# Kernel optimization log

Hardware: AMD Instinct MI355X
Metric: run time of the kernel (lower is better)

The kernel has to match this reference:

```python
import jax, jax.numpy as jnp
import numpy as np
from fractions import Fraction
from math import factorial, sqrt

# ---------- e3nn-convention real Wigner 3j, unit Frobenius norm ----------
def _su2_cg(j1, m1, j2, m2, j3, m3):
    if m3 != m1 + m2:
        return 0.0
    f = lambda n: factorial(int(n))
    vmin = int(max(-j1 + j2 + m3, -j1 + m1, 0))
    vmax = int(min(j2 + j3 + m1, j3 - j1 + j2, j3 + m3))
    C = ((2.0 * j3 + 1.0) * Fraction(
        f(j3 + j1 - j2) * f(j3 - j1 + j2) * f(j1 + j2 - j3) * f(j3 + m3) * f(j3 - m3),
        f(j1 + j2 + j3 + 1) * f(j1 - m1) * f(j1 + m1) * f(j2 - m2) * f(j2 + m2))) ** 0.5
    S = Fraction(0)
    for v in range(vmin, vmax + 1):
        S += (-1) ** int(v + j2 + m2) * Fraction(
            f(j2 + j3 + m1 - v) * f(j1 - m1 + v),
            f(v) * f(j3 - j1 + j2 - v) * f(j3 + m3 - v) * f(v + j1 - j2 - m3))
    return float(C) * float(S)

def _q(l):  # real->complex spherical-harmonic change of basis (e3nn convention)
    q = np.zeros((2 * l + 1, 2 * l + 1), dtype=np.complex128)
    for m in range(-l, 0):
        q[l + m, l + abs(m)] = 1 / 2 ** 0.5
        q[l + m, l - abs(m)] = -1j / 2 ** 0.5
    q[l, l] = 1
    for m in range(1, l + 1):
        q[l + m, l + abs(m)] = (-1) ** m / 2 ** 0.5
        q[l + m, l - abs(m)] = 1j * (-1) ** m / 2 ** 0.5
    return (-1j) ** l * q

def wigner_3j(l1, l2, l3):
    cg = np.zeros((2 * l1 + 1, 2 * l2 + 1, 2 * l3 + 1))
    for m1 in range(-l1, l1 + 1):
        for m2 in range(-l2, l2 + 1):
            if abs(m1 + m2) <= l3:
                cg[l1 + m1, l2 + m2, l3 + m1 + m2] = _su2_cg(l1, m1, l2, m2, l3, m1 + m2)
    C = np.einsum('ij,kl,mn,ikn->jlm', _q(l1), _q(l2), np.conj(_q(l3).T), cg.astype(np.complex128))
    C = np.real(C)
    return (C / np.linalg.norm(C)).astype(np.float32)

# ---------- TensorProduct config: 32x0e+32x1o+32x2e (x) same -> same, all uvw paths ----------
MUL = 32
LS = (0, 1, 2)
OFF = (0, MUL * 1, MUL * 1 + MUL * 3)  # block offsets in the flat 288-dim layout
DIM = MUL * (1 + 3 + 5)                # 288
INS = [(0, 0, 0), (1, 1, 0), (2, 2, 0),
       (0, 1, 1), (1, 0, 1), (1, 2, 1), (2, 1, 1),
       (0, 2, 2), (1, 1, 2), (2, 0, 2), (2, 2, 2)]
_counts = {io: sum(1 for i in INS if i[2] == io) for io in set(i[2] for i in INS)}
# 'component' normalization: scale unit-norm w3j by sqrt(2*l_out+1); uvw mode: alpha=sqrt(path_weight/(n_paths_to_out*mul1*mul2))
ALPHA = [sqrt((2 * LS[io] + 1) / (_counts[io] * MUL * MUL)) for (_, _, io) in INS]
W3J = {(LS[i1], LS[i2], LS[io]): wigner_3j(LS[i1], LS[i2], LS[io]) for (i1, i2, io) in INS}


def setup_inputs() -> dict:
    key = jax.random.key(0)
    k1, k2, k3 = jax.random.split(key, 3)
    B = 2048
    return {
        'x1': jax.random.normal(k1, (B, DIM), dtype=jnp.float32),
        'x2': jax.random.normal(k2, (B, DIM), dtype=jnp.float32),
        'ws': jax.random.normal(k3, (len(INS), MUL, MUL, MUL), dtype=jnp.float32),
    }


def reference(x1, x2, ws):
    B = x1.shape[0]
    out = jnp.zeros((B, DIM), dtype=x1.dtype)
    for p, (i1, i2, io) in enumerate(INS):
        l1, l2, lo = LS[i1], LS[i2], LS[io]
        s1 = x1[:, OFF[i1]:OFF[i1] + MUL * (2 * l1 + 1)].reshape(B, MUL, 2 * l1 + 1)
        s2 = x2[:, OFF[i2]:OFF[i2] + MUL * (2 * l2 + 1)].reshape(B, MUL, 2 * l2 + 1)
        C = jnp.asarray(W3J[(l1, l2, lo)], dtype=x1.dtype)
        # z u v w: batch, mul_in1, mul_in2, mul_out ; i j k: 2l+1 components
        r = jnp.einsum('uvw,ijk,zui,zvj->zwk', ws[p], C, s1, s2)
        out = out.at[:, OFF[io]:OFF[io] + MUL * (2 * lo + 1)].add(ALPHA[p] * r.reshape(B, -1))
    return out
```

## Files before the change

### kernel.cpp

```cpp
#include <hip/hip_runtime.h>
#include <hip/hip_bf16.h>
#include <cmath>
#include <complex>
#include <algorithm>


typedef std::complex<double> cd;

static double factd(int n) { double r = 1; for (int i = 2; i <= n; ++i) r *= i; return r; }

static double su2_cg(int j1, int m1, int j2, int m2, int j3, int m3) {
    if (m3 != m1 + m2) return 0.0;
    int vmin = std::max(std::max(-j1 + j2 + m3, -j1 + m1), 0);
    int vmax = std::min(std::min(j2 + j3 + m1, j3 - j1 + j2), j3 + m3);
    double C = std::sqrt((2.0 * j3 + 1.0) *
        (factd(j3 + j1 - j2) * factd(j3 - j1 + j2) * factd(j1 + j2 - j3) *
         factd(j3 + m3) * factd(j3 - m3)) /
        (factd(j1 + j2 + j3 + 1) * factd(j1 - m1) * factd(j1 + m1) *
         factd(j2 - m2) * factd(j2 + m2)));
    double S = 0.0;
    for (int v = vmin; v <= vmax; ++v) {
        double sgn = ((v + j2 + m2) & 1) ? -1.0 : 1.0;
        S += sgn * (factd(j2 + j3 + m1 - v) * factd(j1 - m1 + v)) /
             (factd(v) * factd(j3 - j1 + j2 - v) * factd(j3 + m3 - v) *
              factd(v + j1 - j2 - m3));
    }
    return C * S;
}

static void qmat(int l, cd* q) {
    int n = 2 * l + 1;
    for (int i = 0; i < n * n; ++i) q[i] = cd(0, 0);
    const double s = 1.0 / std::sqrt(2.0);
    for (int m = -l; m < 0; ++m) {
        q[(l + m) * n + (l - m)] = cd(s, 0);
        q[(l + m) * n + (l + m)] = cd(0, -s);
    }
    q[l * n + l] = cd(1, 0);
    for (int m = 1; m <= l; ++m) {
        double sg = (m & 1) ? -1.0 : 1.0;
        q[(l + m) * n + (l + m)] = cd(sg * s, 0);
        q[(l + m) * n + (l - m)] = cd(0, sg * s);
    }
    cd ph(1, 0);
    for (int t = 0; t < l; ++t) ph *= cd(0, -1);
    for (int i = 0; i < n * n; ++i) q[i] *= ph;
}

static void wigner3j_dense(int l1, int l2, int l3, double* outp) {
    int n1 = 2 * l1 + 1, n2 = 2 * l2 + 1, n3 = 2 * l3 + 1;
    double cg[125];
    for (int i = 0; i < n1 * n2 * n3; ++i) cg[i] = 0.0;
    for (int m1 = -l1; m1 <= l1; ++m1)
        for (int m2 = -l2; m2 <= l2; ++m2) {
            int m3 = m1 + m2;
            if (std::abs(m3) <= l3)
                cg[((l1 + m1) * n2 + (l2 + m2)) * n3 + (l3 + m3)] =
                    su2_cg(l1, m1, l2, m2, l3, m3);
        }
    cd q1[25], q2[25], q3[25];
    qmat(l1, q1); qmat(l2, q2); qmat(l3, q3);
    double norm2 = 0.0;
    for (int j = 0; j < n1; ++j)
        for (int l = 0; l < n2; ++l)
            for (int m = 0; m < n3; ++m) {
                cd sum(0, 0);
                for (int i = 0; i < n1; ++i)
                    for (int k = 0; k < n2; ++k)
                        for (int n = 0; n < n3; ++n) {
                            double g = cg[(i * n2 + k) * n3 + n];
                            if (g != 0.0)
                                sum += q1[i * n1 + j] * q2[k * n2 + l] *
                                       std::conj(q3[n * n3 + m]) * g;
                        }
                outp[(j * n2 + l) * n3 + m] = sum.real();
                norm2 += sum.real() * sum.real();
            }
    double inv = 1.0 / std::sqrt(norm2);
    for (int t = 0; t < n1 * n2 * n3; ++t) outp[t] *= inv;
}


struct E3 { unsigned char i, j, k; };

constexpr E3 PAT_P0[1]  = {{0,0,0}};
constexpr E3 PAT_P1[3]  = {{0,0,0},{1,1,0},{2,2,0}};
constexpr E3 PAT_P2[5]  = {{0,0,0},{1,1,0},{2,2,0},{3,3,0},{4,4,0}};
constexpr E3 PAT_P3[3]  = {{0,0,0},{0,1,1},{0,2,2}};
constexpr E3 PAT_P4[3]  = {{0,0,0},{1,0,1},{2,0,2}};
constexpr E3 PAT_P5[11] = {{1,2,1},{1,3,2},{1,1,0},{2,2,2},{0,2,0},{2,3,1},
                           {0,1,1},{2,4,2},{0,0,2},{2,0,0},{0,4,0}};
constexpr E3 PAT_P6[11] = {{2,1,1},{2,2,2},{2,0,0},{3,1,2},{1,1,0},{3,2,1},
                           {1,0,1},{4,2,2},{0,0,2},{4,0,0},{0,2,0}};
constexpr E3 PAT_P7[5]  = {{0,0,0},{0,1,1},{0,2,2},{0,3,3},{0,4,4}};
constexpr E3 PAT_P8[11] = {{1,1,2},{1,2,3},{1,0,1},{2,1,3},{0,1,1},{2,2,2},
                           {0,0,2},{2,2,4},{0,0,4},{2,0,0},{0,2,0}};
constexpr E3 PAT_P9[5]  = {{0,0,0},{1,0,1},{2,0,2},{3,0,3},{4,0,4}};
constexpr E3 PAT_P10[25]= {{2,2,2},{2,3,3},{2,1,1},{2,4,4},{2,0,0},{3,2,3},
                           {1,2,1},{3,3,2},{1,1,2},{3,3,4},{1,1,4},{3,1,0},
                           {1,3,0},{3,4,3},{1,0,3},{3,0,1},{1,4,1},{4,2,4},
                           {0,2,0},{4,3,3},{0,1,3},{4,1,1},{0,3,1},{4,4,2},
                           {0,0,2}};

constexpr int OFF_P[11] = {0, 1, 4, 9, 12, 15, 26, 37, 42, 53, 58};

struct W3JArg { float c[83]; };

static W3JArg build_w3j_sparse() {
    struct PD { const E3* pat; int ne; int l1, l2, lo; double alpha; };
    const double a0 = std::sqrt(1.0/3072.0), a1 = std::sqrt(3.0/4096.0),
                 a2 = std::sqrt(5.0/4096.0);
    const PD pd[11] = {
        {PAT_P0, 1, 0,0,0, a0}, {PAT_P1, 3, 1,1,0, a0}, {PAT_P2, 5, 2,2,0, a0},
        {PAT_P3, 3, 0,1,1, a1}, {PAT_P4, 3, 1,0,1, a1}, {PAT_P5,11, 1,2,1, a1},
        {PAT_P6,11, 2,1,1, a1}, {PAT_P7, 5, 0,2,2, a2}, {PAT_P8,11, 1,1,2, a2},
        {PAT_P9, 5, 2,0,2, a2}, {PAT_P10,25,2,2,2, a2}
    };
    W3JArg arg;
    for (int p = 0; p < 11; ++p) {
        double dense[125];
        wigner3j_dense(pd[p].l1, pd[p].l2, pd[p].lo, dense);
        int n2 = 2*pd[p].l2+1, n3 = 2*pd[p].lo+1;
        for (int e = 0; e < pd[p].ne; ++e) {
            const E3& t = pd[p].pat[e];
            arg.c[OFF_P[p] + e] =
                (float)(dense[(t.i * n2 + t.j) * n3 + t.k] * pd[p].alpha);
        }
    }
    return arg;
}


typedef __attribute__((ext_vector_type(8))) short short8;
typedef __attribute__((ext_vector_type(4))) float f32x4;

__device__ __forceinline__ unsigned short f2bf_bits(float f) {
    __hip_bfloat16 h = __float2bfloat16(f);
    unsigned short u; __builtin_memcpy(&u, &h, 2); return u;
}

__device__ __forceinline__ unsigned pack2(float lo, float hi) {
    float2 f2; f2.x = lo; f2.y = hi;
    __hip_bfloat162 pk = __float22bfloat162_rn(f2);
    unsigned u; __builtin_memcpy(&u, &pk, 4); return u;
}

template<int NE, int A1, int A2, int D3, int SBASE, int SSTR>
__device__ __forceinline__ void do_path(const E3 (&pat)[NE],
                                        const float* __restrict__ cs,
                                        const float* a, const float* b0,
                                        const float* b1,
                                        unsigned* __restrict__ dst) {
    float ca[NE];
    #pragma unroll
    for (int e = 0; e < NE; ++e) ca[e] = cs[e] * a[A1 + pat[e].i];
    float t0[D3], t1[D3];
    #pragma unroll
    for (int k = 0; k < D3; ++k) { t0[k] = 0.0f; t1[k] = 0.0f; }
    #pragma unroll
    for (int e = 0; e < NE; ++e) {
        const int k = pat[e].k;
        t0[k] = fmaf(ca[e], b0[A2 + pat[e].j], t0[k]);
        t1[k] = fmaf(ca[e], b1[A2 + pat[e].j], t1[k]);
    }
    #pragma unroll
    for (int k = 0; k < D3; ++k)
        dst[(SBASE + k * SSTR) * 256] = pack2(t0[k], t1[k]);
}

__device__ __forceinline__ void build_all(const float* __restrict__ cs,
                                          const float* a, const float* b0,
                                          const float* b1,
                                          unsigned* __restrict__ dst) {
    do_path< 1,0,0,1, 0,1>(PAT_P0,  cs +  0, a, b0, b1, dst);
    do_path< 3,1,1,1, 1,1>(PAT_P1,  cs +  1, a, b0, b1, dst);
    do_path< 5,4,4,1, 2,1>(PAT_P2,  cs +  4, a, b0, b1, dst);
    do_path< 3,0,1,3, 3,4>(PAT_P3,  cs +  9, a, b0, b1, dst);
    do_path< 3,1,0,3, 4,4>(PAT_P4,  cs + 12, a, b0, b1, dst);
    do_path<11,1,4,3, 5,4>(PAT_P5,  cs + 15, a, b0, b1, dst);
    do_path<11,4,1,3, 6,4>(PAT_P6,  cs + 26, a, b0, b1, dst);
    do_path< 5,0,4,5,15,4>(PAT_P7,  cs + 37, a, b0, b1, dst);
    do_path<11,1,1,5,16,4>(PAT_P8,  cs + 42, a, b0, b1, dst);
    do_path< 5,4,0,5,17,4>(PAT_P9,  cs + 53, a, b0, b1, dst);
    do_path<25,4,4,5,18,4>(PAT_P10, cs + 58, a, b0, b1, dst);
}

__device__ __forceinline__ void load_a(const float* __restrict__ x1r, int u,
                                       float* a) {
    a[0] = x1r[u];
    #pragma unroll
    for (int i = 0; i < 3; ++i) a[1 + i] = x1r[32 + u * 3 + i];
    #pragma unroll
    for (int i = 0; i < 5; ++i) a[4 + i] = x1r[128 + u * 5 + i];
}

template<bool USE_WST>
__device__ __forceinline__ short8 load_bfrag(const float* __restrict__ ws,
                                             const unsigned short* __restrict__ wsT,
                                             int p, int u, int w, int vbase) {
    if constexpr (USE_WST) {
        return *(const short8*)(wsT + (((size_t)(p*32+u)*32 + w)*32 + vbase));
    } else {
        short8 r;
        #pragma unroll
        for (int j = 0; j < 8; ++j) {
            float f = ws[((size_t)(p*32+u)*32 + (vbase+j))*32 + w];
            r[j] = (short)f2bf_bits(f);
        }
        return r;
    }
}

__global__ void ws_prep(const float* __restrict__ ws,
                        unsigned short* __restrict__ wsT) {
    __shared__ float tile[32][33];
    const int pu = blockIdx.x, tid = threadIdx.x;
    const float4 f = ((const float4*)(ws + (size_t)pu * 1024))[tid];
    const int v = tid >> 3, w0 = (tid & 7) * 4;
    tile[v][w0+0] = f.x; tile[v][w0+1] = f.y; tile[v][w0+2] = f.z; tile[v][w0+3] = f.w;
    __syncthreads();
    const int w = tid >> 3, vB = (tid & 7) * 4;
    ushort4 o;
    o.x = f2bf_bits(tile[vB+0][w]); o.y = f2bf_bits(tile[vB+1][w]);
    o.z = f2bf_bits(tile[vB+2][w]); o.w = f2bf_bits(tile[vB+3][w]);
    *(ushort4*)(wsT + (size_t)pu * 1024 + tid * 4) = o;
}


__launch_bounds__(256, 4)
__global__ void tp_mfma(const float* __restrict__ x1,
                        const float* __restrict__ x2,
                        const unsigned short* __restrict__ wsT,
                        float* __restrict__ part, int ZT, W3JArg w3j) {
    __shared__ unsigned shT[35 * 256];

    const int tid = threadIdx.x;
    const int l = tid & 63, wv = tid >> 6, kh = wv & 1, nt = wv >> 1;
    const int zt = blockIdx.x & (ZT - 1);
    const int ug = blockIdx.x / ZT;
    const int z0 = zt * 16, u0 = ug * 4;
    const int tz = tid >> 4, vp = tid & 15, v0 = vp * 2;

    float b0[9], b1[9];
    {
        const float* xr = x2 + (size_t)(z0 + tz) * 288;
        float2 s0 = *(const float2*)(xr + v0);
        b0[0] = s0.x; b1[0] = s0.y;
        const float* p1 = xr + 32 + v0 * 3;
        float2 q0 = *(const float2*)(p1 + 0);
        float2 q1 = *(const float2*)(p1 + 2);
        float2 q2 = *(const float2*)(p1 + 4);
        b0[1] = q0.x; b0[2] = q0.y; b0[3] = q1.x;
        b1[1] = q1.y; b1[2] = q2.x; b1[3] = q2.y;
        const float* p2 = xr + 128 + v0 * 5;
        #pragma unroll
        for (int h = 0; h < 5; ++h) {
            float2 r = *(const float2*)(p2 + 2 * h);
            if (2 * h < 5) b0[4 + 2 * h] = r.x; else b1[4 + 2 * h - 5] = r.x;
            if (2 * h + 1 < 5) b0[5 + 2 * h] = r.y; else b1[4 + 2 * h - 4] = r.y;
        }
    }

    const float* x1r = x1 + (size_t)(z0 + tz) * 288;

    unsigned* dstT = shT + tz * 16 + (vp & 3) + ((((vp >> 2) + (tz >> 1)) & 3) << 2);
    const unsigned* tbase = shT + (l & 15) * 16 +
                            ((((l >> 4) + ((l & 15) >> 1)) & 3) << 2);

    const int w  = (l & 15) + nt * 16;
    const int vb = (l >> 4) * 8;

    f32x4 acc[5];
    #pragma unroll
    for (int i = 0; i < 5; ++i) acc[i] = (f32x4)(0.0f);

    float a[2][9];
    load_a(x1r, u0, a[0]);

    for (int ui = 0; ui < 4; ++ui) {
        const int u = u0 + ui;
        const int cur = ui & 1;

        __syncthreads();

        short8 bf[7];
        if (kh == 0) {
            #pragma unroll
            for (int p = 0; p < 7; ++p) bf[p] = load_bfrag<true>(nullptr, wsT, p, u, w, vb);
        } else {
            #pragma unroll
            for (int p = 0; p < 4; ++p) bf[p] = load_bfrag<true>(nullptr, wsT, 7 + p, u, w, vb);
        }
        if (ui < 3) load_a(x1r, u + 1, a[cur ^ 1]);

        build_all(w3j.c, a[cur], b0, b1, dstT);
        __syncthreads();

        if (kh == 0) {
            #pragma unroll
            for (int m = 0; m < 3; ++m) {
                short8 af = *(const short8*)(tbase + m * 256);
                acc[0] = __builtin_amdgcn_mfma_f32_16x16x32_bf16(af, bf[m], acc[0], 0, 0, 0);
            }
            #pragma unroll
            for (int g = 0; g < 3; ++g)
                #pragma unroll
                for (int m = 0; m < 4; ++m) {
                    short8 af = *(const short8*)(tbase + (3 + g*4 + m) * 256);
                    acc[1+g] = __builtin_amdgcn_mfma_f32_16x16x32_bf16(af, bf[3+m], acc[1+g], 0, 0, 0);
                }
        } else {
            #pragma unroll
            for (int g = 0; g < 5; ++g)
                #pragma unroll
                for (int m = 0; m < 4; ++m) {
                    short8 af = *(const short8*)(tbase + (15 + g*4 + m) * 256);
                    acc[g] = __builtin_amdgcn_mfma_f32_16x16x32_bf16(af, bf[m], acc[g], 0, 0, 0);
                }
        }
    }

    float* pb = part + ((size_t)(ug * ZT + zt) * 9) * 512;
    const int zi4 = (l >> 4) << 2;
    if (kh == 0) {
        #pragma unroll
        for (int r = 0; r < 4; ++r)
            pb[(zi4 + r) * 32 + w] = acc[0][r];
        #pragma unroll
        for (int k = 0; k < 3; ++k)
            #pragma unroll
            for (int r = 0; r < 4; ++r)
                pb[(1 + k) * 512 + (zi4 + r) * 32 + w] = acc[1 + k][r];
    } else {
        #pragma unroll
        for (int k = 0; k < 5; ++k)
            #pragma unroll
            for (int r = 0; r < 4; ++r)
                pb[(4 + k) * 512 + (zi4 + r) * 32 + w] = acc[k][r];
    }
}


__global__ void reduce_out(const float* __restrict__ part,
                           float* __restrict__ out, int ZT) {
    const int bid = blockIdx.x;
    const int zt = bid / 9, comp = bid - zt * 9;
    const int tid = threadIdx.x;
    #pragma unroll
    for (int h = 0; h < 2; ++h) {
        const int e = tid + h * 256;
        const int zi = e >> 5, w = e & 31;
        float s = 0.0f;
        #pragma unroll
        for (int g = 0; g < 8; ++g)
            s += part[((size_t)(g * ZT + zt) * 9 + comp) * 512 + e];
        int col;
        if (comp == 0)      col = w;
        else if (comp < 4)  col = 32 + w * 3 + (comp - 1);
        else                col = 128 + w * 5 + (comp - 4);
        out[(size_t)(zt * 16 + zi) * 288 + col] = s;
    }
}


__launch_bounds__(256, 4)
__global__ void tp_mfma_atomic(const float* __restrict__ x1,
                               const float* __restrict__ x2,
                               const float* __restrict__ ws,
                               float* __restrict__ out, int ZT, W3JArg w3j) {
    __shared__ unsigned shT[35 * 256];
    const int tid = threadIdx.x;
    const int l = tid & 63, wv = tid >> 6, kh = wv & 1, nt = wv >> 1;
    const int zt = blockIdx.x & (ZT - 1);
    const int ug = blockIdx.x / ZT;
    const int z0 = zt * 16, u0 = ug * 4;
    const int tz = tid >> 4, vp = tid & 15, v0 = vp * 2;

    float b0[9], b1[9];
    {
        const float* xr = x2 + (size_t)(z0 + tz) * 288;
        float2 s0 = *(const float2*)(xr + v0);
        b0[0] = s0.x; b1[0] = s0.y;
        const float* p1 = xr + 32 + v0 * 3;
        float2 q0 = *(const float2*)(p1 + 0);
        float2 q1 = *(const float2*)(p1 + 2);
        float2 q2 = *(const float2*)(p1 + 4);
        b0[1] = q0.x; b0[2] = q0.y; b0[3] = q1.x;
        b1[1] = q1.y; b1[2] = q2.x; b1[3] = q2.y;
        const float* p2 = xr + 128 + v0 * 5;
        #pragma unroll
        for (int h = 0; h < 5; ++h) {
            float2 r = *(const float2*)(p2 + 2 * h);
            if (2 * h < 5) b0[4 + 2 * h] = r.x; else b1[4 + 2 * h - 5] = r.x;
            if (2 * h + 1 < 5) b0[5 + 2 * h] = r.y; else b1[4 + 2 * h - 4] = r.y;
        }
    }
    const float* x1r = x1 + (size_t)(z0 + tz) * 288;
    unsigned* dstT = shT + tz * 16 + (vp & 3) + ((((vp >> 2) + (tz >> 1)) & 3) << 2);
    const unsigned* tbase = shT + (l & 15) * 16 +
                            ((((l >> 4) + ((l & 15) >> 1)) & 3) << 2);
    const int w  = (l & 15) + nt * 16;
    const int vb = (l >> 4) * 8;

    f32x4 acc[5];
    #pragma unroll
    for (int i = 0; i < 5; ++i) acc[i] = (f32x4)(0.0f);
    float a[2][9];
    load_a(x1r, u0, a[0]);

    for (int ui = 0; ui < 4; ++ui) {
        const int u = u0 + ui;
        const int cur = ui & 1;
        __syncthreads();
        short8 bf[7];
        if (kh == 0) {
            #pragma unroll
            for (int p = 0; p < 7; ++p) bf[p] = load_bfrag<false>(ws, nullptr, p, u, w, vb);
        } else {
            #pragma unroll
            for (int p = 0; p < 4; ++p) bf[p] = load_bfrag<false>(ws, nullptr, 7 + p, u, w, vb);
        }
        if (ui < 3) load_a(x1r, u + 1, a[cur ^ 1]);
        build_all(w3j.c, a[cur], b0, b1, dstT);
        __syncthreads();
        if (kh == 0) {
            #pragma unroll
            for (int m = 0; m < 3; ++m) {
                short8 af = *(const short8*)(tbase + m * 256);
                acc[0] = __builtin_amdgcn_mfma_f32_16x16x32_bf16(af, bf[m], acc[0], 0, 0, 0);
            }
            #pragma unroll
            for (int g = 0; g < 3; ++g)
                #pragma unroll
                for (int m = 0; m < 4; ++m) {
                    short8 af = *(const short8*)(tbase + (3 + g*4 + m) * 256);
                    acc[1+g] = __builtin_amdgcn_mfma_f32_16x16x32_bf16(af, bf[3+m], acc[1+g], 0, 0, 0);
                }
        } else {
            #pragma unroll
            for (int g = 0; g < 5; ++g)
                #pragma unroll
                for (int m = 0; m < 4; ++m) {
                    short8 af = *(const short8*)(tbase + (15 + g*4 + m) * 256);
                    acc[g] = __builtin_amdgcn_mfma_f32_16x16x32_bf16(af, bf[m], acc[g], 0, 0, 0);
                }
        }
    }
    const int zr = z0 + ((l >> 4) << 2);
    if (kh == 0) {
        #pragma unroll
        for (int r = 0; r < 4; ++r)
            atomicAdd(&out[(size_t)(zr + r) * 288 + w], acc[0][r]);
        #pragma unroll
        for (int k = 0; k < 3; ++k)
            #pragma unroll
            for (int r = 0; r < 4; ++r)
                atomicAdd(&out[(size_t)(zr + r) * 288 + 32 + w*3 + k], acc[1+k][r]);
    } else {
        #pragma unroll
        for (int k = 0; k < 5; ++k)
            #pragma unroll
            for (int r = 0; r < 4; ++r)
                atomicAdd(&out[(size_t)(zr + r) * 288 + 128 + w*5 + k], acc[k][r]);
    }
}


extern "C" void kernel_launch(void* const* d_in, const int* in_sizes, int n_in,
                              void* d_out, int out_size, void* d_ws, size_t ws_size,
                              hipStream_t stream) {
    const float* x1 = (const float*)d_in[0];
    const float* x2 = (const float*)d_in[1];
    const float* ws = (const float*)d_in[2];
    float* out = (float*)d_out;

    static const W3JArg arg = build_w3j_sparse();

    const int B = in_sizes[0] / 288;
    const int ZT = B / 16;
    const int grid_main = 8 * ZT;

    const size_t part_off_b = 786432;
    const size_t part_bytes = (size_t)8 * ZT * 9 * 512 * 4;

    if (ws_size >= part_off_b + part_bytes) {
        unsigned short* wsT = (unsigned short*)d_ws;
        float* part = (float*)((char*)d_ws + part_off_b);
        ws_prep<<<dim3(11 * 32), dim3(256), 0, stream>>>(ws, wsT);
        tp_mfma<<<dim3(grid_main), dim3(256), 0, stream>>>(x1, x2, wsT, part, ZT, arg);
        reduce_out<<<dim3(ZT * 9), dim3(256), 0, stream>>>(part, out, ZT);
    } else {
        hipMemsetAsync(out, 0, (size_t)out_size * sizeof(float), stream);
        tp_mfma_atomic<<<dim3(grid_main), dim3(256), 0, stream>>>(x1, x2, ws, out, ZT, arg);
    }
}
```

Before: 88.61 us.

## Build MFMA A-fragments in registers with fp16 packed math, one wave per block

The main kernel now gives each wave its own block and builds the Wigner-contracted A fragments directly in registers using packed half2 FMAs. This removes the shared-memory staging and the two __syncthreads per u step. Weights are converted to fp16 instead of bf16 and the MFMA switches to the f16 variant. The risks are heavy register pressure from the held x2 half2 values and fully unrolled slot builds, and fp16 precision or overflow in the intermediate products.

```diff
diff --git a/kernel.cpp b/kernel.cpp
--- a/kernel.cpp
+++ b/kernel.cpp
@@ -1,7 +1,9 @@
 #include <hip/hip_runtime.h>
 #include <hip/hip_bf16.h>
+#include <hip/hip_fp16.h>
 #include <cmath>
 #include <complex>
+#include <cstring>
 #include <algorithm>
 
 
@@ -104,9 +106,23 @@
 
 constexpr int OFF_P[11] = {0, 1, 4, 9, 12, 15, 26, 37, 42, 53, 58};
 
-struct W3JArg { float c[83]; };
-
-static W3JArg build_w3j_sparse() {
+struct W3JArg  { float    c[83];  };
+struct W3JHalf { unsigned c2[83]; };
+
+static unsigned short f32_to_f16_bits(float f) {
+    unsigned x; std::memcpy(&x, &f, 4);
+    unsigned sign = (x >> 16) & 0x8000u;
+    int exp = (int)((x >> 23) & 0xff) - 127 + 15;
+    unsigned man = x & 0x7fffffu;
+    if (exp <= 0) return (unsigned short)sign;
+    if (exp >= 31) return (unsigned short)(sign | 0x7c00u);
+    unsigned h = sign | ((unsigned)exp << 10) | (man >> 13);
+    unsigned rem = man & 0x1fffu;
+    if (rem > 0x1000u || (rem == 0x1000u && (h & 1u))) h++;
+    return (unsigned short)h;
+}
+
+static void build_w3j_both(W3JArg& argf, W3JHalf& argh) {
     struct PD { const E3* pat; int ne; int l1, l2, lo; double alpha; };
     const double a0 = std::sqrt(1.0/3072.0), a1 = std::sqrt(3.0/4096.0),
                  a2 = std::sqrt(5.0/4096.0);
@@ -116,22 +132,23 @@
         {PAT_P6,11, 2,1,1, a1}, {PAT_P7, 5, 0,2,2, a2}, {PAT_P8,11, 1,1,2, a2},
         {PAT_P9, 5, 2,0,2, a2}, {PAT_P10,25,2,2,2, a2}
     };
-    W3JArg arg;
     for (int p = 0; p < 11; ++p) {
         double dense[125];
         wigner3j_dense(pd[p].l1, pd[p].l2, pd[p].lo, dense);
         int n2 = 2*pd[p].l2+1, n3 = 2*pd[p].lo+1;
         for (int e = 0; e < pd[p].ne; ++e) {
             const E3& t = pd[p].pat[e];
-            arg.c[OFF_P[p] + e] =
-                (float)(dense[(t.i * n2 + t.j) * n3 + t.k] * pd[p].alpha);
-        }
-    }
-    return arg;
+            float v = (float)(dense[(t.i * n2 + t.j) * n3 + t.k] * pd[p].alpha);
+            argf.c[OFF_P[p] + e] = v;
+            unsigned short hb = f32_to_f16_bits(v);
+            argh.c2[OFF_P[p] + e] = (unsigned)hb | ((unsigned)hb << 16);
+        }
+    }
 }
 
 
 typedef __attribute__((ext_vector_type(8))) short short8;
+typedef __attribute__((ext_vector_type(8))) _Float16 half8;
 typedef __attribute__((ext_vector_type(4))) float f32x4;
 
 __device__ __forceinline__ unsigned short f2bf_bits(float f) {
@@ -144,6 +161,221 @@
     __hip_bfloat162 pk = __float22bfloat162_rn(f2);
     unsigned u; __builtin_memcpy(&u, &pk, 4); return u;
 }
+
+__device__ __forceinline__ void load_a(const float* __restrict__ x1r, int u,
+                                       float* a) {
+    a[0] = x1r[u];
+    #pragma unroll
+    for (int i = 0; i < 3; ++i) a[1 + i] = x1r[32 + u * 3 + i];
+    #pragma unroll
+    for (int i = 0; i < 5; ++i) a[4 + i] = x1r[128 + u * 5 + i];
+}
+
+__global__ void ws_prep(const float* __restrict__ ws,
+                        unsigned short* __restrict__ wsT) {
+    __shared__ float tile[32][33];
+    const int pu = blockIdx.x, tid = threadIdx.x;
+    const float4 f = ((const float4*)(ws + (size_t)pu * 1024))[tid];
+    const int v = tid >> 3, w0 = (tid & 7) * 4;
+    tile[v][w0+0] = f.x; tile[v][w0+1] = f.y; tile[v][w0+2] = f.z; tile[v][w0+3] = f.w;
+    __syncthreads();
+    const int w = tid >> 3, vB = (tid & 7) * 4;
+    ushort4 o;
+    __half h0 = __float2half(tile[vB+0][w]); __builtin_memcpy(&o.x, &h0, 2);
+    __half h1 = __float2half(tile[vB+1][w]); __builtin_memcpy(&o.y, &h1, 2);
+    __half h2 = __float2half(tile[vB+2][w]); __builtin_memcpy(&o.z, &h2, 2);
+    __half h3 = __float2half(tile[vB+3][w]); __builtin_memcpy(&o.w, &h3, 2);
+    *(ushort4*)(wsT + (size_t)pu * 1024 + tid * 4) = o;
+}
+
+
+template<int NE, int K, int A1, int A2>
+__device__ __forceinline__ void build_slot(const E3 (&pat)[NE],
+                                           const unsigned* __restrict__ c2,
+                                           const __half2* a2,
+                                           const __half2 (&b2)[9][4],
+                                           __half2 (&t)[4]) {
+    const __half2 z2 = __float2half2_rn(0.0f);
+    #pragma unroll
+    for (int q = 0; q < 4; ++q) t[q] = z2;
+    #pragma unroll
+    for (int e = 0; e < NE; ++e) {
+        if ((int)pat[e].k == K) {
+            unsigned cb = c2[e];
+            __half2 c; __builtin_memcpy(&c, &cb, 4);
+            __half2 ca = __hmul2(c, a2[A1 + pat[e].i]);
+            #pragma unroll
+            for (int q = 0; q < 4; ++q)
+                t[q] = __hfma2(ca, b2[A2 + pat[e].j][q], t[q]);
+        }
+    }
+}
+
+__device__ __forceinline__ f32x4 mfma_t(const __half2 (&t)[4], half8 bf, f32x4 acc) {
+    half8 af; __builtin_memcpy(&af, &t, 16);
+    return __builtin_amdgcn_mfma_f32_16x16x32_f16(af, bf, acc, 0, 0, 0);
+}
+
+__launch_bounds__(64, 4)
+__global__ void tp_mfma_reg(const float* __restrict__ x1,
+                            const float* __restrict__ x2,
+                            const unsigned short* __restrict__ wsT,
+                            float* __restrict__ part, int ZT, W3JHalf w3j) {
+    const int l = threadIdx.x;
+    const int bx = blockIdx.x;
+    const int zt = bx & (ZT - 1);
+    const int r  = bx / ZT;
+    const int wv = r & 3, ug = r >> 2;
+    const int kh = wv & 1, nt = wv >> 1;
+    const int z0 = zt * 16, u0 = ug * 4;
+
+    const int z  = l & 15;
+    const int vo = (l >> 4) * 8;
+    const int w  = (l & 15) + nt * 16;
+    const int vb = (l >> 4) * 8;
+
+    const float* xr = x2 + (size_t)(z0 + z) * 288;
+    __half2 b2[9][4];
+    {
+        float f0[8];
+        *(float4*)&f0[0] = *(const float4*)(xr + vo);
+        *(float4*)&f0[4] = *(const float4*)(xr + vo + 4);
+        #pragma unroll
+        for (int q = 0; q < 4; ++q)
+            b2[0][q] = __floats2half2_rn(f0[2*q], f0[2*q+1]);
+        float f1[24];
+        #pragma unroll
+        for (int t4 = 0; t4 < 6; ++t4)
+            *(float4*)&f1[4*t4] = *(const float4*)(xr + 32 + 3*vo + 4*t4);
+        #pragma unroll
+        for (int j = 0; j < 3; ++j)
+            #pragma unroll
+            for (int q = 0; q < 4; ++q)
+                b2[1+j][q] = __floats2half2_rn(f1[6*q+j], f1[6*q+3+j]);
+        float f2[40];
+        #pragma unroll
+        for (int t4 = 0; t4 < 10; ++t4)
+            *(float4*)&f2[4*t4] = *(const float4*)(xr + 128 + 5*vo + 4*t4);
+        #pragma unroll
+        for (int j = 0; j < 5; ++j)
+            #pragma unroll
+            for (int q = 0; q < 4; ++q)
+                b2[4+j][q] = __floats2half2_rn(f2[10*q+j], f2[10*q+5+j]);
+    }
+
+    const float* x1r = x1 + (size_t)(z0 + z) * 288;
+    const unsigned* c2 = w3j.c2;
+
+    f32x4 acc[5];
+    #pragma unroll
+    for (int i = 0; i < 5; ++i) acc[i] = (f32x4)(0.0f);
+
+    float a[2][9];
+    load_a(x1r, u0, a[0]);
+
+    for (int ui = 0; ui < 4; ++ui) {
+        const int u = u0 + ui;
+        const int cur = ui & 1;
+
+        half8 bf[7];
+        if (kh == 0) {
+            #pragma unroll
+            for (int p = 0; p < 7; ++p)
+                bf[p] = *(const half8*)(wsT + (((size_t)(p*32+u)*32 + w)*32 + vb));
+        } else {
+            #pragma unroll
+            for (int p = 0; p < 4; ++p)
+                bf[p] = *(const half8*)(wsT + (((size_t)((7+p)*32+u)*32 + w)*32 + vb));
+        }
+        if (ui < 3) load_a(x1r, u + 1, a[cur ^ 1]);
+
+        __half2 a2[9];
+        #pragma unroll
+        for (int i = 0; i < 9; ++i) a2[i] = __float2half2_rn(a[cur][i]);
+
+        __half2 t[4];
+        if (kh == 0) {
+            build_slot< 1,0,0,0>(PAT_P0, c2+0, a2, b2, t);  acc[0] = mfma_t(t, bf[0], acc[0]);
+            build_slot< 3,0,1,1>(PAT_P1, c2+1, a2, b2, t);  acc[0] = mfma_t(t, bf[1], acc[0]);
+            build_slot< 5,0,4,4>(PAT_P2, c2+4, a2, b2, t);  acc[0] = mfma_t(t, bf[2], acc[0]);
+            build_slot< 3,0,0,1>(PAT_P3, c2+ 9, a2, b2, t); acc[1] = mfma_t(t, bf[3], acc[1]);
+            build_slot< 3,0,1,0>(PAT_P4, c2+12, a2, b2, t); acc[1] = mfma_t(t, bf[4], acc[1]);
+            build_slot<11,0,1,4>(PAT_P5, c2+15, a2, b2, t); acc[1] = mfma_t(t, bf[5], acc[1]);
+            build_slot<11,0,4,1>(PAT_P6, c2+26, a2, b2, t); acc[1] = mfma_t(t, bf[6], acc[1]);
+            build_slot< 3,1,0,1>(PAT_P3, c2+ 9, a2, b2, t); acc[2] = mfma_t(t, bf[3], acc[2]);
+            build_slot< 3,1,1,0>(PAT_P4, c2+12, a2, b2, t); acc[2] = mfma_t(t, bf[4], acc[2]);
+            build_slot<11,1,1,4>(PAT_P5, c2+15, a2, b2, t); acc[2] = mfma_t(t, bf[5], acc[2]);
+            build_slot<11,1,4,1>(PAT_P6, c2+26, a2, b2, t); acc[2] = mfma_t(t, bf[6], acc[2]);
+            build_slot< 3,2,0,1>(PAT_P3, c2+ 9, a2, b2, t); acc[3] = mfma_t(t, bf[3], acc[3]);
+            build_slot< 3,2,1,0>(PAT_P4, c2+12, a2, b2, t); acc[3] = mfma_t(t, bf[4], acc[3]);
+            build_slot<11,2,1,4>(PAT_P5, c2+15, a2, b2, t); acc[3] = mfma_t(t, bf[5], acc[3]);
+            build_slot<11,2,4,1>(PAT_P6, c2+26, a2, b2, t); acc[3] = mfma_t(t, bf[6], acc[3]);
+        } else {
+            build_slot< 5,0,0,4>(PAT_P7,  c2+37, a2, b2, t); acc[0] = mfma_t(t, bf[0], acc[0]);
+            build_slot<11,0,1,1>(PAT_P8,  c2+42, a2, b2, t); acc[0] = mfma_t(t, bf[1], acc[0]);
+            build_slot< 5,0,4,0>(PAT_P9,  c2+53, a2, b2, t); acc[0] = mfma_t(t, bf[2], acc[0]);
+            build_slot<25,0,4,4>(PAT_P10, c2+58, a2, b2, t); acc[0] = mfma_t(t, bf[3], acc[0]);
+            build_slot< 5,1,0,4>(PAT_P7,  c2+37, a2, b2, t); acc[1] = mfma_t(t, bf[0], acc[1]);
+            build_slot<11,1,1,1>(PAT_P8,  c2+42, a2, b2, t); acc[1] = mfma_t(t, bf[1], acc[1]);
+            build_slot< 5,1,4,0>(PAT_P9,  c2+53, a2, b2, t); acc[1] = mfma_t(t, bf[2], acc[1]);
+            build_slot<25,1,4,4>(PAT_P10, c2+58, a2, b2, t); acc[1] = mfma_t(t, bf[3], acc[1]);
+            build_slot< 5,2,0,4>(PAT_P7,  c2+37, a2, b2, t); acc[2] = mfma_t(t, bf[0], acc[2]);
+            build_slot<11,2,1,1>(PAT_P8,  c2+42, a2, b2, t); acc[2] = mfma_t(t, bf[1], acc[2]);
+            build_slot< 5,2,4,0>(PAT_P9,  c2+53, a2, b2, t); acc[2] = mfma_t(t, bf[2], acc[2]);
+            build_slot<25,2,4,4>(PAT_P10, c2+58, a2, b2, t); acc[2] = mfma_t(t, bf[3], acc[2]);
+            build_slot< 5,3,0,4>(PAT_P7,  c2+37, a2, b2, t); acc[3] = mfma_t(t, bf[0], acc[3]);
+            build_slot<11,3,1,1>(PAT_P8,  c2+42, a2, b2, t); acc[3] = mfma_t(t, bf[1], acc[3]);
+            build_slot< 5,3,4,0>(PAT_P9,  c2+53, a2, b2, t); acc[3] = mfma_t(t, bf[2], acc[3]);
+            build_slot<25,3,4,4>(PAT_P10, c2+58, a2, b2, t); acc[3] = mfma_t(t, bf[3], acc[3]);
+            build_slot< 5,4,0,4>(PAT_P7,  c2+37, a2, b2, t); acc[4] = mfma_t(t, bf[0], acc[4]);
+            build_slot<11,4,1,1>(PAT_P8,  c2+42, a2, b2, t); acc[4] = mfma_t(t, bf[1], acc[4]);
+            build_slot< 5,4,4,0>(PAT_P9,  c2+53, a2, b2, t); acc[4] = mfma_t(t, bf[2], acc[4]);
+            build_slot<25,4,4,4>(PAT_P10, c2+58, a2, b2, t); acc[4] = mfma_t(t, bf[3], acc[4]);
+        }
+    }
+
+    float* pb = part + ((size_t)(ug * ZT + zt) * 9) * 512;
+    const int zi4 = (l >> 4) << 2;
+    if (kh == 0) {
+        #pragma unroll
+        for (int rr = 0; rr < 4; ++rr)
+            pb[(zi4 + rr) * 32 + w] = acc[0][rr];
+        #pragma unroll
+        for (int k = 0; k < 3; ++k)
+            #pragma unroll
+            for (int rr = 0; rr < 4; ++rr)
+                pb[(1 + k) * 512 + (zi4 + rr) * 32 + w] = acc[1 + k][rr];
+    } else {
+        #pragma unroll
+        for (int k = 0; k < 5; ++k)
+            #pragma unroll
+            for (int rr = 0; rr < 4; ++rr)
+                pb[(4 + k) * 512 + (zi4 + rr) * 32 + w] = acc[k][rr];
+    }
+}
+
+
+__global__ void reduce_out(const float* __restrict__ part,
+                           float* __restrict__ out, int ZT) {
+    const int bid = blockIdx.x;
+    const int zt = bid / 9, comp = bid - zt * 9;
+    const int tid = threadIdx.x;
+    #pragma unroll
+    for (int h = 0; h < 2; ++h) {
+        const int e = tid + h * 256;
+        const int zi = e >> 5, w = e & 31;
+        float s = 0.0f;
+        #pragma unroll
+        for (int g = 0; g < 8; ++g)
+            s += part[((size_t)(g * ZT + zt) * 9 + comp) * 512 + e];
+        int col;
+        if (comp == 0)      col = w;
+        else if (comp < 4)  col = 32 + w * 3 + (comp - 1);
+        else                col = 128 + w * 5 + (comp - 4);
+        out[(size_t)(zt * 16 + zi) * 288 + col] = s;
+    }
+}
+
 
 template<int NE, int A1, int A2, int D3, int SBASE, int SSTR>
 __device__ __forceinline__ void do_path(const E3 (&pat)[NE],
@@ -185,55 +417,23 @@
     do_path<25,4,4,5,18,4>(PAT_P10, cs + 58, a, b0, b1, dst);
 }
 
-__device__ __forceinline__ void load_a(const float* __restrict__ x1r, int u,
-                                       float* a) {
-    a[0] = x1r[u];
-    #pragma unroll
-    for (int i = 0; i < 3; ++i) a[1 + i] = x1r[32 + u * 3 + i];
-    #pragma unroll
-    for (int i = 0; i < 5; ++i) a[4 + i] = x1r[128 + u * 5 + i];
-}
-
-template<bool USE_WST>
-__device__ __forceinline__ short8 load_bfrag(const float* __restrict__ ws,
-                                             const unsigned short* __restrict__ wsT,
-                                             int p, int u, int w, int vbase) {
-    if constexpr (USE_WST) {
-        return *(const short8*)(wsT + (((size_t)(p*32+u)*32 + w)*32 + vbase));
-    } else {
-        short8 r;
-        #pragma unroll
-        for (int j = 0; j < 8; ++j) {
-            float f = ws[((size_t)(p*32+u)*32 + (vbase+j))*32 + w];
-            r[j] = (short)f2bf_bits(f);
-        }
-        return r;
-    }
-}
-
-__global__ void ws_prep(const float* __restrict__ ws,
-                        unsigned short* __restrict__ wsT) {
-    __shared__ float tile[32][33];
-    const int pu = blockIdx.x, tid = threadIdx.x;
-    const float4 f = ((const float4*)(ws + (size_t)pu * 1024))[tid];
-    const int v = tid >> 3, w0 = (tid & 7) * 4;
-    tile[v][w0+0] = f.x; tile[v][w0+1] = f.y; tile[v][w0+2] = f.z; tile[v][w0+3] = f.w;
-    __syncthreads();
-    const int w = tid >> 3, vB = (tid & 7) * 4;
-    ushort4 o;
-    o.x = f2bf_bits(tile[vB+0][w]); o.y = f2bf_bits(tile[vB+1][w]);
-    o.z = f2bf_bits(tile[vB+2][w]); o.w = f2bf_bits(tile[vB+3][w]);
-    *(ushort4*)(wsT + (size_t)pu * 1024 + tid * 4) = o;
-}
-
+__device__ __forceinline__ short8 load_bfrag_f32(const float* __restrict__ ws,
+                                                 int p, int u, int w, int vbase) {
+    short8 r;
+    #pragma unroll
+    for (int j = 0; j < 8; ++j) {
+        float f = ws[((size_t)(p*32+u)*32 + (vbase+j))*32 + w];
+        r[j] = (short)f2bf_bits(f);
+    }
+    return r;
+}
 
 __launch_bounds__(256, 4)
-__global__ void tp_mfma(const float* __restrict__ x1,
-                        const float* __restrict__ x2,
-                        const unsigned short* __restrict__ wsT,
-                        float* __restrict__ part, int ZT, W3JArg w3j) {
+__global__ void tp_mfma_atomic(const float* __restrict__ x1,
+                               const float* __restrict__ x2,
+                               const float* __restrict__ ws,
+                               float* __restrict__ out, int ZT, W3JArg w3j) {
     __shared__ unsigned shT[35 * 256];
-
     const int tid = threadIdx.x;
     const int l = tid & 63, wv = tid >> 6, kh = wv & 1, nt = wv >> 1;
     const int zt = blockIdx.x & (ZT - 1);
@@ -260,42 +460,34 @@
             if (2 * h + 1 < 5) b0[5 + 2 * h] = r.y; else b1[4 + 2 * h - 4] = r.y;
         }
     }
-
     const float* x1r = x1 + (size_t)(z0 + tz) * 288;
-
     unsigned* dstT = shT + tz * 16 + (vp & 3) + ((((vp >> 2) + (tz >> 1)) & 3) << 2);
     const unsigned* tbase = shT + (l & 15) * 16 +
                             ((((l >> 4) + ((l & 15) >> 1)) & 3) << 2);
-
     const int w  = (l & 15) + nt * 16;
     const int vb = (l >> 4) * 8;
 
     f32x4 acc[5];
     #pragma unroll
     for (int i = 0; i < 5; ++i) acc[i] = (f32x4)(0.0f);
-
     float a[2][9];
     load_a(x1r, u0, a[0]);
 
     for (int ui = 0; ui < 4; ++ui) {
         const int u = u0 + ui;
         const int cur = ui & 1;
-
         __syncthreads();
-
         short8 bf[7];
         if (kh == 0) {
             #pragma unroll
-            for (int p = 0; p < 7; ++p) bf[p] = load_bfrag<true>(nullptr, wsT, p, u, w, vb);
+            for (int p = 0; p < 7; ++p) bf[p] = load_bfrag_f32(ws, p, u, w, vb);
         } else {
             #pragma unroll
-            for (int p = 0; p < 4; ++p) bf[p] = load_bfrag<true>(nullptr, wsT, 7 + p, u, w, vb);
+            for (int p = 0; p < 4; ++p) bf[p] = load_bfrag_f32(ws, 7 + p, u, w, vb);
         }
         if (ui < 3) load_a(x1r, u + 1, a[cur ^ 1]);
-
         build_all(w3j.c, a[cur], b0, b1, dstT);
         __syncthreads();
-
         if (kh == 0) {
             #pragma unroll
             for (int m = 0; m < 3; ++m) {
@@ -319,149 +511,22 @@
                 }
         }
     }
-
-    float* pb = part + ((size_t)(ug * ZT + zt) * 9) * 512;
-    const int zi4 = (l >> 4) << 2;
-    if (kh == 0) {
-        #pragma unroll
-        for (int r = 0; r < 4; ++r)
-            pb[(zi4 + r) * 32 + w] = acc[0][r];
-        #pragma unroll
-        for (int k = 0; k < 3; ++k)
-            #pragma unroll
-            for (int r = 0; r < 4; ++r)
-                pb[(1 + k) * 512 + (zi4 + r) * 32 + w] = acc[1 + k][r];
-    } else {
-        #pragma unroll
-        for (int k = 0; k < 5; ++k)
-            #pragma unroll
-            for (int r = 0; r < 4; ++r)
-                pb[(4 + k) * 512 + (zi4 + r) * 32 + w] = acc[k][r];
-    }
-}
-
-
-__global__ void reduce_out(const float* __restrict__ part,
-                           float* __restrict__ out, int ZT) {
-    const int bid = blockIdx.x;
-    const int zt = bid / 9, comp = bid - zt * 9;
-    const int tid = threadIdx.x;
-    #pragma unroll
-    for (int h = 0; h < 2; ++h) {
-        const int e = tid + h * 256;
-        const int zi = e >> 5, w = e & 31;
-        float s = 0.0f;
-        #pragma unroll
-        for (int g = 0; g < 8; ++g)
-            s += part[((size_t)(g * ZT + zt) * 9 + comp) * 512 + e];
-        int col;
-        if (comp == 0)      col = w;
-        else if (comp < 4)  col = 32 + w * 3 + (comp - 1);
-        else                col = 128 + w * 5 + (comp - 4);
-        out[(size_t)(zt * 16 + zi) * 288 + col] = s;
-    }
-}
-
-
-__launch_bounds__(256, 4)
-__global__ void tp_mfma_atomic(const float* __restrict__ x1,
-                               const float* __restrict__ x2,
-                               const float* __restrict__ ws,
-                               float* __restrict__ out, int ZT, W3JArg w3j) {
-    __shared__ unsigned shT[35 * 256];
-    const int tid = threadIdx.x;
-    const int l = tid & 63, wv = tid >> 6, kh = wv & 1, nt = wv >> 1;
-    const int zt = blockIdx.x & (ZT - 1);
-    const int ug = blockIdx.x / ZT;
-    const int z0 = zt * 16, u0 = ug * 4;
-    const int tz = tid >> 4, vp = tid & 15, v0 = vp * 2;
-
-    float b0[9], b1[9];
-    {
-        const float* xr = x2 + (size_t)(z0 + tz) * 288;
-        float2 s0 = *(const float2*)(xr + v0);
-        b0[0] = s0.x; b1[0] = s0.y;
-        const float* p1 = xr + 32 + v0 * 3;
-        float2 q0 = *(const float2*)(p1 + 0);
-        float2 q1 = *(const float2*)(p1 + 2);
-        float2 q2 = *(const float2*)(p1 + 4);
-        b0[1] = q0.x; b0[2] = q0.y; b0[3] = q1.x;
-        b1[1] = q1.y; b1[2] = q2.x; b1[3] = q2.y;
-        const float* p2 = xr + 128 + v0 * 5;
-        #pragma unroll
-        for (int h = 0; h < 5; ++h) {
-            float2 r = *(const float2*)(p2 + 2 * h);
-            if (2 * h < 5) b0[4 + 2 * h] = r.x; else b1[4 + 2 * h - 5] = r.x;
-            if (2 * h + 1 < 5) b0[5 + 2 * h] = r.y; else b1[4 + 2 * h - 4] = r.y;
-        }
-    }
-    const float* x1r = x1 + (size_t)(z0 + tz) * 288;
-    unsigned* dstT = shT + tz * 16 + (vp & 3) + ((((vp >> 2) + (tz >> 1)) & 3) << 2);
-    const unsigned* tbase = shT + (l & 15) * 16 +
-                            ((((l >> 4) + ((l & 15) >> 1)) & 3) << 2);
-    const int w  = (l & 15) + nt * 16;
-    const int vb = (l >> 4) * 8;
-
-    f32x4 acc[5];
-    #pragma unroll
-    for (int i = 0; i < 5; ++i) acc[i] = (f32x4)(0.0f);
-    float a[2][9];
-    load_a(x1r, u0, a[0]);
-
-    for (int ui = 0; ui < 4; ++ui) {
-        const int u = u0 + ui;
-        const int cur = ui & 1;
-        __syncthreads();
-        short8 bf[7];
-        if (kh == 0) {
-            #pragma unroll
-            for (int p = 0; p < 7; ++p) bf[p] = load_bfrag<false>(ws, nullptr, p, u, w, vb);
-        } else {
-            #pragma unroll
-            for (int p = 0; p < 4; ++p) bf[p] = load_bfrag<false>(ws, nullptr, 7 + p, u, w, vb);
-        }
-        if (ui < 3) load_a(x1r, u + 1, a[cur ^ 1]);
-        build_all(w3j.c, a[cur], b0, b1, dstT);
-        __syncthreads();
-        if (kh == 0) {
-            #pragma unroll
-            for (int m = 0; m < 3; ++m) {
-                short8 af = *(const short8*)(tbase + m * 256);
-                acc[0] = __builtin_amdgcn_mfma_f32_16x16x32_bf16(af, bf[m], acc[0], 0, 0, 0);
-            }
-            #pragma unroll
-            for (int g = 0; g < 3; ++g)
-                #pragma unroll
-                for (int m = 0; m < 4; ++m) {
-                    short8 af = *(const short8*)(tbase + (3 + g*4 + m) * 256);
-                    acc[1+g] = __builtin_amdgcn_mfma_f32_16x16x32_bf16(af, bf[3+m], acc[1+g], 0, 0, 0);
-                }
-        } else {
-            #pragma unroll
-            for (int g = 0; g < 5; ++g)
-                #pragma unroll
-                for (int m = 0; m < 4; ++m) {
-                    short8 af = *(const short8*)(tbase + (15 + g*4 + m) * 256);
-                    acc[g] = __builtin_amdgcn_mfma_f32_16x16x32_bf16(af, bf[m], acc[g], 0, 0, 0);
-                }
-        }
-    }
     const int zr = z0 + ((l >> 4) << 2);
     if (kh == 0) {
         #pragma unroll
-        for (int r = 0; r < 4; ++r)
-            atomicAdd(&out[(size_t)(zr + r) * 288 + w], acc[0][r]);
+        for (int rr = 0; rr < 4; ++rr)
+            atomicAdd(&out[(size_t)(zr + rr) * 288 + w], acc[0][rr]);
         #pragma unroll
         for (int k = 0; k < 3; ++k)
             #pragma unroll
-            for (int r = 0; r < 4; ++r)
-                atomicAdd(&out[(size_t)(zr + r) * 288 + 32 + w*3 + k], acc[1+k][r]);
+            for (int rr = 0; rr < 4; ++rr)
+                atomicAdd(&out[(size_t)(zr + rr) * 288 + 32 + w*3 + k], acc[1+k][rr]);
     } else {
         #pragma unroll
         for (int k = 0; k < 5; ++k)
             #pragma unroll
-            for (int r = 0; r < 4; ++r)
-                atomicAdd(&out[(size_t)(zr + r) * 288 + 128 + w*5 + k], acc[k][r]);
+            for (int rr = 0; rr < 4; ++rr)
+                atomicAdd(&out[(size_t)(zr + rr) * 288 + 128 + w*5 + k], acc[k][rr]);
     }
 }
 
@@ -474,11 +539,11 @@
     const float* ws = (const float*)d_in[2];
     float* out = (float*)d_out;
 
-    static const W3JArg arg = build_w3j_sparse();
+    static W3JArg argf; static W3JHalf argh; static bool init = false;
+    if (!init) { build_w3j_both(argf, argh); init = true; }
 
     const int B = in_sizes[0] / 288;
     const int ZT = B / 16;
-    const int grid_main = 8 * ZT;
 
     const size_t part_off_b = 786432;
     const size_t part_bytes = (size_t)8 * ZT * 9 * 512 * 4;
@@ -487,10 +552,10 @@
         unsigned short* wsT = (unsigned short*)d_ws;
         float* part = (float*)((char*)d_ws + part_off_b);
         ws_prep<<<dim3(11 * 32), dim3(256), 0, stream>>>(ws, wsT);
-        tp_mfma<<<dim3(grid_main), dim3(256), 0, stream>>>(x1, x2, wsT, part, ZT, arg);
+        tp_mfma_reg<<<dim3(32 * ZT), dim3(64), 0, stream>>>(x1, x2, wsT, part, ZT, argh);
         reduce_out<<<dim3(ZT * 9), dim3(256), 0, stream>>>(part, out, ZT);
     } else {
         hipMemsetAsync(out, 0, (size_t)out_size * sizeof(float), stream);
-        tp_mfma_atomic<<<dim3(grid_main), dim3(256), 0, stream>>>(x1, x2, ws, out, ZT, arg);
-    }
-}
+        tp_mfma_atomic<<<dim3(8 * ZT), dim3(256), 0, stream>>>(x1, x2, ws, out, ZT, argf);
+    }
+}
```

Measured after the change: 100.4 us. 13.3% more time.
